# Performance work log

Measured on AMD Instinct MI355X. Metric: run time of the kernel, lower is better.

Reference implementation:

```python
import jax, jax.numpy as jnp
import numpy as np

B, N, D = 16, 2048, 128
NEG = jnp.float32(-2.0**32 + 1)

def setup_inputs() -> dict:
    key = jax.random.key(0)
    ks = jax.random.split(key, 9)
    s = 1.0 / np.sqrt(D)
    return {
        "queries": jax.random.normal(ks[0], (B, N, D), jnp.float32),
        "keys": jax.random.normal(ks[1], (B, N, D), jnp.float32),
        "padding_mask": jax.random.randint(ks[2], (B, N), 0, 2, jnp.int32),
        "Wq": jax.random.uniform(ks[3], (D, D), jnp.float32, -s, s),
        "bq": jax.random.uniform(ks[4], (D,), jnp.float32, -s, s),
        "Wk": jax.random.uniform(ks[5], (D, D), jnp.float32, -s, s),
        "bk": jax.random.uniform(ks[6], (D,), jnp.float32, -s, s),
        "Wv": jax.random.uniform(ks[7], (D, D), jnp.float32, -s, s),
        "bv": jax.random.uniform(ks[8], (D,), jnp.float32, -s, s),
    }

def reference(queries, keys, padding_mask, Wq, bq, Wk, bk, Wv, bv):
    d = queries.shape[-1]
    eq = queries @ Wq.T + bq            # [B,N,D]
    ek = keys @ Wk.T + bk               # [B,N,D]
    ev = keys @ Wv.T + bv               # [B,N,D]
    # scaled scores [B,N,N]
    coefs = jnp.einsum('bnd,bmd->bnm', eq, ek) / jnp.sqrt(jnp.float32(d))
    # key padding: large negative where keys row sums to zero (broadcast over query axis)
    key_pad = (jnp.sum(keys, axis=-1) == 0).astype(jnp.float32) * NEG   # [B,N]
    out = jnp.where(padding_mask[:, None, :] == 0, key_pad[:, None, :], coefs)
    out = jax.nn.softmax(out, axis=2)
    # NOTE: original applies query mask along the KEY axis (unsqueeze(1)) -- kept faithfully
    q_pad = (jnp.sum(queries, axis=-1) != 0).astype(jnp.float32)        # [B,N]
    out = out * q_pad[:, None, :]
    out = jnp.einsum('bnm,bmd->bnd', out, ev)
    return out + queries
```

## Files before the change

kernel.cpp:

```cpp
#include <hip/hip_runtime.h>
#include <hip/hip_bf16.h>


#define SCALE_LOG2E 0.12751875f

typedef __bf16 bf16x8 __attribute__((ext_vector_type(8)));
typedef float  f32x4  __attribute__((ext_vector_type(4)));

static __device__ __forceinline__ float fexp2(float x) {
#if __has_builtin(__builtin_amdgcn_exp2f)
    return __builtin_amdgcn_exp2f(x);
#else
    float r; asm("v_exp_f32 %0, %1" : "=v"(r) : "v"(x)); return r;
#endif
}

__global__ __launch_bounds__(256) void prep_kernel(
    const float* __restrict__ Wq, const float* __restrict__ Wk,
    const float* __restrict__ Wv, __bf16* __restrict__ wb)
{
    int i = blockIdx.x * 256 + threadIdx.x;
    int w = i >> 11, c = i & 2047;
    int col = c & 15, quad = (c >> 4) & 3, f = (c >> 6) & 3, ct = c >> 8;
    const float* src = ((w == 0) ? Wq : (w == 1) ? Wk : Wv)
                       + (size_t)(ct * 16 + col) * 128 + f * 32 + quad * 8;
    float4 a = *(const float4*)src, b = *(const float4*)(src + 4);
    bf16x8 t = {(__bf16)a.x, (__bf16)a.y, (__bf16)a.z, (__bf16)a.w,
                (__bf16)b.x, (__bf16)b.y, (__bf16)b.z, (__bf16)b.w};
    *(bf16x8*)&wb[(size_t)w * 16384 + (size_t)c * 8] = t;
}

__global__ __launch_bounds__(256) void proj_kernel(
    const float* __restrict__ Q, const float* __restrict__ K,
    const int* __restrict__ PM, const __bf16* __restrict__ wb,
    const float* __restrict__ Bq, const float* __restrict__ Bk,
    const float* __restrict__ Bv,
    __bf16* __restrict__ eqb, __bf16* __restrict__ ekf, __bf16* __restrict__ evf,
    float* __restrict__ madd)
{
    __shared__ __bf16 stage[128 * 72];
    const int tid  = threadIdx.x;
    const int wave = tid >> 6, lane = tid & 63;
    const int col  = lane & 15, quad = lane >> 4;
    const int w = blockIdx.x >> 9;
    const int rowbase = (blockIdx.x & 511) * 64;
    const int myrow   = rowbase + wave * 16 + col;
    const int bb   = rowbase >> 11;
    const int m16b = (rowbase & 2047) >> 4;

    const float* asrc = (w == 0) ? Q : K;
    bf16x8 a[4];
    float ss = 0.f;
    #pragma unroll
    for (int f = 0; f < 4; ++f) {
        const float* p = asrc + (size_t)myrow * 128 + f * 32 + quad * 8;
        float4 v0 = *(const float4*)p, v1 = *(const float4*)(p + 4);
        float vv[8] = {v0.x, v0.y, v0.z, v0.w, v1.x, v1.y, v1.z, v1.w};
        #pragma unroll
        for (int j = 0; j < 8; ++j) { ss += vv[j]; a[f][j] = (__bf16)vv[j]; }
    }

    float rm = 1.f;
    if (w == 1) {
        ss += __shfl_xor(ss, 16); ss += __shfl_xor(ss, 32);
        int pmv = PM[myrow];
        rm = (pmv != 0) ? 1.f : 0.f;
        if (quad == 0) madd[myrow] = (pmv == 0 && ss == 0.f) ? -1.0e5f : 0.f;
    } else if (w == 2) {
        float qs = 0.f;
        #pragma unroll
        for (int f = 0; f < 4; ++f) {
            const float* p = Q + (size_t)myrow * 128 + f * 32 + quad * 8;
            float4 v0 = *(const float4*)p, v1 = *(const float4*)(p + 4);
            qs += v0.x + v0.y + v0.z + v0.w + v1.x + v1.y + v1.z + v1.w;
        }
        qs += __shfl_xor(qs, 16); qs += __shfl_xor(qs, 32);
        rm = (qs != 0.f) ? 1.f : 0.f;
    }
    float rmul[4];
    #pragma unroll
    for (int r = 0; r < 4; ++r) rmul[r] = __shfl(rm, quad * 4 + r);

    const float sc = (w == 0) ? SCALE_LOG2E : 1.f;
    const float* bias = (w == 0) ? Bq : (w == 1) ? Bk : Bv;
    const __bf16* wbp = wb + w * 16384;

    f32x4 acc[8];
    #pragma unroll
    for (int ct = 0; ct < 8; ++ct) { f32x4 z = {0.f, 0.f, 0.f, 0.f}; acc[ct] = z; }
    #pragma unroll
    for (int f = 0; f < 4; ++f) {
        #pragma unroll
        for (int ct = 0; ct < 8; ++ct) {
            bf16x8 bfr = *(const bf16x8*)&wbp[(size_t)(ct * 4 + f) * 512 + lane * 8];
            acc[ct] = __builtin_amdgcn_mfma_f32_16x16x32_bf16(a[f], bfr, acc[ct], 0, 0, 0);
        }
    }
    #pragma unroll
    for (int ct = 0; ct < 8; ++ct) {
        float bv = bias[ct * 16 + col];
        #pragma unroll
        for (int r = 0; r < 4; ++r) {
            float v = (acc[ct][r] + bv) * rmul[r] * sc;
            int rr = wave * 16 + quad * 4 + r;
            if (w == 2) stage[(ct * 16 + col) * 72 + rr] = (__bf16)v;
            else        stage[rr * 136 + ct * 16 + col] = (__bf16)v;
        }
    }
    __syncthreads();

    if (w == 0) {
        int r = tid >> 2, seg = (tid & 3) * 32;
        uint4* g4 = (uint4*)(eqb + (size_t)(rowbase + r) * 128 + seg);
        const uint4* s4 = (const uint4*)&stage[r * 136 + seg];
        g4[0] = s4[0]; g4[1] = s4[1]; g4[2] = s4[2]; g4[3] = s4[3];
    } else if (w == 1) {
        __bf16* dst = ekf + (size_t)bb * 2048 * 128 + (size_t)m16b * 2048;
        #pragma unroll
        for (int c = 0; c < 4; ++c) {
            int s = tid + c * 256;
            int l = s & 63, f = (s >> 6) & 3, m = s >> 8;
            *(uint4*)&dst[(size_t)s * 8] =
                *(const uint4*)&stage[(m * 16 + (l & 15)) * 136 + f * 32 + ((l >> 4) & 3) * 8];
        }
    } else {
        __bf16* dst = evf + (size_t)bb * 2048 * 128 + (size_t)(rowbase & 2047) * 128;
        #pragma unroll
        for (int c = 0; c < 4; ++c) {
            int s = tid + c * 256;
            int l = s & 63, dt = (s >> 6) & 7, tl = s >> 9;
            int cl = l & 15, ql = l >> 4;
            uint2 xa = *(const uint2*)&stage[(dt * 16 + cl) * 72 + tl * 32 + ql * 4];
            uint2 xb = *(const uint2*)&stage[(dt * 16 + cl) * 72 + tl * 32 + 16 + ql * 4];
            uint4 v = {xa.x, xa.y, xb.x, xb.y};
            *(uint4*)&dst[(size_t)s * 8] = v;
        }
    }
}

__global__ __launch_bounds__(256, 2) void attn_kernel(
    const __bf16* __restrict__ eqb, const __bf16* __restrict__ ekf,
    const __bf16* __restrict__ evf, const float* __restrict__ madd,
    const float* __restrict__ Q, float* __restrict__ out)
{
    __shared__ struct { float obuf[2][32 * 140]; float lbuf[2][32]; } sm;

    const int tid  = threadIdx.x;
    const int wave = tid >> 6, lane = tid & 63;
    const int col  = lane & 15, quad = lane >> 4;
    const int i  = blockIdx.x;
    const int b  = 2 * (i & 7) + ((i >> 3) & 1);
    const int qt = i >> 4;
    const int rowg0 = b * 2048 + qt * 32;
    const __bf16* ekb_b = ekf + (size_t)b * 2048 * 128;
    const __bf16* evb_b = evf + (size_t)b * 2048 * 128;
    const float*  dmb   = madd + b * 2048;

    bf16x8 aqf[2][4];
    #pragma unroll
    for (int q2 = 0; q2 < 2; ++q2)
        #pragma unroll
        for (int f = 0; f < 4; ++f)
            aqf[q2][f] = *(const bf16x8*)&eqb[(size_t)(rowg0 + q2 * 16 + col) * 128 + f * 32 + quad * 8];

    f32x4 o[2][8];
    float lsum[2] = {0.f, 0.f};
    #pragma unroll
    for (int q2 = 0; q2 < 2; ++q2)
        #pragma unroll
        for (int dt = 0; dt < 8; ++dt) { f32x4 z = {0.f, 0.f, 0.f, 0.f}; o[q2][dt] = z; }

    const int kq0 = wave * 512;

    bf16x8 kc[8], vf[8];
    {
        const int m16 = kq0 >> 4;
        #pragma unroll
        for (int f = 0; f < 4; ++f) {
            kc[f]     = *(const bf16x8*)&ekb_b[(size_t)((m16 + 0) * 4 + f) * 512 + lane * 8];
            kc[4 + f] = *(const bf16x8*)&ekb_b[(size_t)((m16 + 1) * 4 + f) * 512 + lane * 8];
        }
        const int t32 = kq0 >> 5;
        #pragma unroll
        for (int dt = 0; dt < 8; ++dt)
            vf[dt] = *(const bf16x8*)&evb_b[((size_t)t32 * 8 + dt) * 512 + lane * 8];
    }
    float4 dm0 = *(const float4*)&dmb[kq0 + quad * 4];
    float4 dm1 = *(const float4*)&dmb[kq0 + 16 + quad * 4];

    for (int it = 0; it < 16; ++it) {
        const int kb = kq0 + it * 32;

        bf16x8 kn[8], vn[8];
        float4 dn0, dn1;
        if (it < 15) {
            const int m16n = (kb >> 4) + 2;
            #pragma unroll
            for (int f = 0; f < 4; ++f) {
                kn[f]     = *(const bf16x8*)&ekb_b[(size_t)((m16n + 0) * 4 + f) * 512 + lane * 8];
                kn[4 + f] = *(const bf16x8*)&ekb_b[(size_t)((m16n + 1) * 4 + f) * 512 + lane * 8];
            }
            const int t32n = (kb >> 5) + 1;
            #pragma unroll
            for (int dt = 0; dt < 8; ++dt)
                vn[dt] = *(const bf16x8*)&evb_b[((size_t)t32n * 8 + dt) * 512 + lane * 8];
            dn0 = *(const float4*)&dmb[kb + 32 + quad * 4];
            dn1 = *(const float4*)&dmb[kb + 48 + quad * 4];
        }

        f32x4 s[2][2];
        {
            f32x4 i0 = {dm0.x, dm0.y, dm0.z, dm0.w};
            f32x4 i1 = {dm1.x, dm1.y, dm1.z, dm1.w};
            s[0][0] = i0; s[0][1] = i1; s[1][0] = i0; s[1][1] = i1;
        }
        __builtin_amdgcn_s_setprio(1);
        #pragma unroll
        for (int f = 0; f < 4; ++f) {
            #pragma unroll
            for (int q2 = 0; q2 < 2; ++q2) {
                s[q2][0] = __builtin_amdgcn_mfma_f32_16x16x32_bf16(kc[f],     aqf[q2][f], s[q2][0], 0, 0, 0);
                s[q2][1] = __builtin_amdgcn_mfma_f32_16x16x32_bf16(kc[4 + f], aqf[q2][f], s[q2][1], 0, 0, 0);
            }
        }
        __builtin_amdgcn_s_setprio(0);

        bf16x8 pq[2];
        #pragma unroll
        for (int q2 = 0; q2 < 2; ++q2)
            #pragma unroll
            for (int g = 0; g < 2; ++g)
                #pragma unroll
                for (int r = 0; r < 4; ++r) {
                    float e = fexp2(s[q2][g][r]);
                    pq[q2][g * 4 + r] = (__bf16)e;
                    lsum[q2] += e;
                }

        __builtin_amdgcn_s_setprio(1);
        #pragma unroll
        for (int dt = 0; dt < 8; ++dt) {
            #pragma unroll
            for (int q2 = 0; q2 < 2; ++q2)
                o[q2][dt] = __builtin_amdgcn_mfma_f32_16x16x32_bf16(vf[dt], pq[q2], o[q2][dt], 0, 0, 0);
        }
        __builtin_amdgcn_s_setprio(0);

        if (it < 15) {
            #pragma unroll
            for (int f = 0; f < 8; ++f) { kc[f] = kn[f]; vf[f] = vn[f]; }
            dm0 = dn0; dm1 = dn1;
        }
    }

    #pragma unroll
    for (int q2 = 0; q2 < 2; ++q2) {
        lsum[q2] += __shfl_xor(lsum[q2], 16);
        lsum[q2] += __shfl_xor(lsum[q2], 32);
    }

    if (wave & 1) {
        int slot = wave >> 1;
        #pragma unroll
        for (int q2 = 0; q2 < 2; ++q2) {
            #pragma unroll
            for (int dt = 0; dt < 8; ++dt) {
                float4 v = {o[q2][dt][0], o[q2][dt][1], o[q2][dt][2], o[q2][dt][3]};
                *(float4*)&sm.obuf[slot][(q2 * 16 + col) * 140 + dt * 16 + quad * 4] = v;
            }
            if (quad == 0) sm.lbuf[slot][q2 * 16 + col] = lsum[q2];
        }
    }
    __syncthreads();
    if (!(wave & 1)) {
        int slot = wave >> 1;
        #pragma unroll
        for (int q2 = 0; q2 < 2; ++q2) {
            lsum[q2] += sm.lbuf[slot][q2 * 16 + col];
            #pragma unroll
            for (int dt = 0; dt < 8; ++dt) {
                float4 t = *(const float4*)&sm.obuf[slot][(q2 * 16 + col) * 140 + dt * 16 + quad * 4];
                o[q2][dt][0] += t.x; o[q2][dt][1] += t.y;
                o[q2][dt][2] += t.z; o[q2][dt][3] += t.w;
            }
        }
    }
    __syncthreads();
    if (wave == 2) {
        #pragma unroll
        for (int q2 = 0; q2 < 2; ++q2) {
            #pragma unroll
            for (int dt = 0; dt < 8; ++dt) {
                float4 v = {o[q2][dt][0], o[q2][dt][1], o[q2][dt][2], o[q2][dt][3]};
                *(float4*)&sm.obuf[0][(q2 * 16 + col) * 140 + dt * 16 + quad * 4] = v;
            }
            if (quad == 0) sm.lbuf[0][q2 * 16 + col] = lsum[q2];
        }
    }
    __syncthreads();
    if (wave == 0) {
        #pragma unroll
        for (int q2 = 0; q2 < 2; ++q2) {
            float inv = 1.f / (lsum[q2] + sm.lbuf[0][q2 * 16 + col]);
            const size_t rowoff = (size_t)(rowg0 + q2 * 16 + col) * 128;
            #pragma unroll
            for (int dt = 0; dt < 8; ++dt) {
                float4 t = *(const float4*)&sm.obuf[0][(q2 * 16 + col) * 140 + dt * 16 + quad * 4];
                f32x4 qres = __builtin_nontemporal_load((const f32x4*)&Q[rowoff + dt * 16 + quad * 4]);
                f32x4 v;
                v[0] = (o[q2][dt][0] + t.x) * inv + qres[0];
                v[1] = (o[q2][dt][1] + t.y) * inv + qres[1];
                v[2] = (o[q2][dt][2] + t.z) * inv + qres[2];
                v[3] = (o[q2][dt][3] + t.w) * inv + qres[3];
                __builtin_nontemporal_store(v, (f32x4*)&out[rowoff + dt * 16 + quad * 4]);
            }
        }
    }
}

extern "C" void kernel_launch(void* const* d_in, const int* in_sizes, int n_in,
                              void* d_out, int out_size, void* d_ws, size_t ws_size,
                              hipStream_t stream)
{
    const float* Q  = (const float*)d_in[0];
    const float* K  = (const float*)d_in[1];
    const int*   PM = (const int*)d_in[2];
    const float* Wq = (const float*)d_in[3];
    const float* Bq = (const float*)d_in[4];
    const float* Wk = (const float*)d_in[5];
    const float* Bk = (const float*)d_in[6];
    const float* Wv = (const float*)d_in[7];
    const float* Bv = (const float*)d_in[8];
    float* out = (float*)d_out;

    const size_t SZE = (size_t)16 * 2048 * 128;
    __bf16* eqb = (__bf16*)d_ws;
    __bf16* ekf = eqb + SZE;
    __bf16* evf = ekf + SZE;
    float* madd = (float*)(evf + SZE);
    __bf16* wb  = (__bf16*)(madd + 16 * 2048);

    prep_kernel<<<24, 256, 0, stream>>>(Wq, Wk, Wv, wb);
    proj_kernel<<<1536, 256, 0, stream>>>(Q, K, PM, wb, Bq, Bk, Bv,
                                          eqb, ekf, evf, madd);
    attn_kernel<<<1024, 256, 0, stream>>>(eqb, ekf, evf, madd, Q, out);
}
```

Baseline: 160.4 us.

## Fuse Q/K/V projections per block and cut attention register and LDS use

The projection kernel now has each block compute the Q, K and V projections for its 64 rows, rather than launching separate blocks per weight. This reads Q and K once and avoids reloading Q for the query-padding check. The attention kernel drops register double-buffering of V fragments, loading them at the start of each iteration instead, and shrinks the LDS reduction buffer to a single slot with a serialized reduction order. The aim is less global traffic and lower register/LDS pressure for better occupancy, at the cost of exposing V load latency and adding more barriers.

New measurement: 165.8 us. 1.03x slower.

```diff
diff --git a/kernel.cpp b/kernel.cpp
--- a/kernel.cpp
+++ b/kernel.cpp
@@ -42,79 +42,88 @@
     const int tid  = threadIdx.x;
     const int wave = tid >> 6, lane = tid & 63;
     const int col  = lane & 15, quad = lane >> 4;
-    const int w = blockIdx.x >> 9;
-    const int rowbase = (blockIdx.x & 511) * 64;
+    const int rowbase = blockIdx.x * 64;
     const int myrow   = rowbase + wave * 16 + col;
     const int bb   = rowbase >> 11;
     const int m16b = (rowbase & 2047) >> 4;
 
-    const float* asrc = (w == 0) ? Q : K;
-    bf16x8 a[4];
-    float ss = 0.f;
+    bf16x8 aq[4], ak[4];
+    float qs = 0.f, ks = 0.f;
     #pragma unroll
     for (int f = 0; f < 4; ++f) {
-        const float* p = asrc + (size_t)myrow * 128 + f * 32 + quad * 8;
+        const float* p = Q + (size_t)myrow * 128 + f * 32 + quad * 8;
         float4 v0 = *(const float4*)p, v1 = *(const float4*)(p + 4);
         float vv[8] = {v0.x, v0.y, v0.z, v0.w, v1.x, v1.y, v1.z, v1.w};
         #pragma unroll
-        for (int j = 0; j < 8; ++j) { ss += vv[j]; a[f][j] = (__bf16)vv[j]; }
-    }
-
-    float rm = 1.f;
-    if (w == 1) {
-        ss += __shfl_xor(ss, 16); ss += __shfl_xor(ss, 32);
-        int pmv = PM[myrow];
-        rm = (pmv != 0) ? 1.f : 0.f;
-        if (quad == 0) madd[myrow] = (pmv == 0 && ss == 0.f) ? -1.0e5f : 0.f;
-    } else if (w == 2) {
-        float qs = 0.f;
-        #pragma unroll
-        for (int f = 0; f < 4; ++f) {
-            const float* p = Q + (size_t)myrow * 128 + f * 32 + quad * 8;
-            float4 v0 = *(const float4*)p, v1 = *(const float4*)(p + 4);
-            qs += v0.x + v0.y + v0.z + v0.w + v1.x + v1.y + v1.z + v1.w;
-        }
-        qs += __shfl_xor(qs, 16); qs += __shfl_xor(qs, 32);
-        rm = (qs != 0.f) ? 1.f : 0.f;
-    }
-    float rmul[4];
-    #pragma unroll
-    for (int r = 0; r < 4; ++r) rmul[r] = __shfl(rm, quad * 4 + r);
-
-    const float sc = (w == 0) ? SCALE_LOG2E : 1.f;
-    const float* bias = (w == 0) ? Bq : (w == 1) ? Bk : Bv;
-    const __bf16* wbp = wb + w * 16384;
-
-    f32x4 acc[8];
-    #pragma unroll
-    for (int ct = 0; ct < 8; ++ct) { f32x4 z = {0.f, 0.f, 0.f, 0.f}; acc[ct] = z; }
-    #pragma unroll
-    for (int f = 0; f < 4; ++f) {
+        for (int j = 0; j < 8; ++j) { qs += vv[j]; aq[f][j] = (__bf16)vv[j]; }
+        const float* pk = K + (size_t)myrow * 128 + f * 32 + quad * 8;
+        float4 w0 = *(const float4*)pk, w1 = *(const float4*)(pk + 4);
+        float ww[8] = {w0.x, w0.y, w0.z, w0.w, w1.x, w1.y, w1.z, w1.w};
+        #pragma unroll
+        for (int j = 0; j < 8; ++j) { ks += ww[j]; ak[f][j] = (__bf16)ww[j]; }
+    }
+    qs += __shfl_xor(qs, 16); qs += __shfl_xor(qs, 32);
+    ks += __shfl_xor(ks, 16); ks += __shfl_xor(ks, 32);
+    int pmv = PM[myrow];
+    if (quad == 0) madd[myrow] = (pmv == 0 && ks == 0.f) ? -1.0e5f : 0.f;
+    float rmk_s = (pmv != 0) ? 1.f : 0.f;
+    float rmv_s = (qs != 0.f) ? 1.f : 0.f;
+    float rk[4], rv[4];
+    #pragma unroll
+    for (int r = 0; r < 4; ++r) {
+        rk[r] = __shfl(rmk_s, quad * 4 + r);
+        rv[r] = __shfl(rmv_s, quad * 4 + r);
+    }
+
+    {
+        f32x4 acc[8];
+        #pragma unroll
+        for (int ct = 0; ct < 8; ++ct) { f32x4 z = {0.f, 0.f, 0.f, 0.f}; acc[ct] = z; }
+        #pragma unroll
+        for (int f = 0; f < 4; ++f)
+            #pragma unroll
+            for (int ct = 0; ct < 8; ++ct) {
+                bf16x8 bfr = *(const bf16x8*)&wb[(size_t)(ct * 4 + f) * 512 + lane * 8];
+                acc[ct] = __builtin_amdgcn_mfma_f32_16x16x32_bf16(aq[f], bfr, acc[ct], 0, 0, 0);
+            }
         #pragma unroll
         for (int ct = 0; ct < 8; ++ct) {
-            bf16x8 bfr = *(const bf16x8*)&wbp[(size_t)(ct * 4 + f) * 512 + lane * 8];
-            acc[ct] = __builtin_amdgcn_mfma_f32_16x16x32_bf16(a[f], bfr, acc[ct], 0, 0, 0);
-        }
-    }
-    #pragma unroll
-    for (int ct = 0; ct < 8; ++ct) {
-        float bv = bias[ct * 16 + col];
-        #pragma unroll
-        for (int r = 0; r < 4; ++r) {
-            float v = (acc[ct][r] + bv) * rmul[r] * sc;
-            int rr = wave * 16 + quad * 4 + r;
-            if (w == 2) stage[(ct * 16 + col) * 72 + rr] = (__bf16)v;
-            else        stage[rr * 136 + ct * 16 + col] = (__bf16)v;
-        }
-    }
-    __syncthreads();
-
-    if (w == 0) {
+            float bvv = Bq[ct * 16 + col];
+            #pragma unroll
+            for (int r = 0; r < 4; ++r) {
+                int rr = wave * 16 + quad * 4 + r;
+                stage[rr * 136 + ct * 16 + col] = (__bf16)((acc[ct][r] + bvv) * SCALE_LOG2E);
+            }
+        }
+        __syncthreads();
         int r = tid >> 2, seg = (tid & 3) * 32;
         uint4* g4 = (uint4*)(eqb + (size_t)(rowbase + r) * 128 + seg);
         const uint4* s4 = (const uint4*)&stage[r * 136 + seg];
         g4[0] = s4[0]; g4[1] = s4[1]; g4[2] = s4[2]; g4[3] = s4[3];
-    } else if (w == 1) {
+    }
+    __syncthreads();
+
+    {
+        f32x4 acc[8];
+        #pragma unroll
+        for (int ct = 0; ct < 8; ++ct) { f32x4 z = {0.f, 0.f, 0.f, 0.f}; acc[ct] = z; }
+        #pragma unroll
+        for (int f = 0; f < 4; ++f)
+            #pragma unroll
+            for (int ct = 0; ct < 8; ++ct) {
+                bf16x8 bfr = *(const bf16x8*)&wb[(size_t)16384 + (size_t)(ct * 4 + f) * 512 + lane * 8];
+                acc[ct] = __builtin_amdgcn_mfma_f32_16x16x32_bf16(ak[f], bfr, acc[ct], 0, 0, 0);
+            }
+        #pragma unroll
+        for (int ct = 0; ct < 8; ++ct) {
+            float bvv = Bk[ct * 16 + col];
+            #pragma unroll
+            for (int r = 0; r < 4; ++r) {
+                int rr = wave * 16 + quad * 4 + r;
+                stage[rr * 136 + ct * 16 + col] = (__bf16)((acc[ct][r] + bvv) * rk[r]);
+            }
+        }
+        __syncthreads();
         __bf16* dst = ekf + (size_t)bb * 2048 * 128 + (size_t)m16b * 2048;
         #pragma unroll
         for (int c = 0; c < 4; ++c) {
@@ -123,7 +132,30 @@
             *(uint4*)&dst[(size_t)s * 8] =
                 *(const uint4*)&stage[(m * 16 + (l & 15)) * 136 + f * 32 + ((l >> 4) & 3) * 8];
         }
-    } else {
+    }
+    __syncthreads();
+
+    {
+        f32x4 acc[8];
+        #pragma unroll
+        for (int ct = 0; ct < 8; ++ct) { f32x4 z = {0.f, 0.f, 0.f, 0.f}; acc[ct] = z; }
+        #pragma unroll
+        for (int f = 0; f < 4; ++f)
+            #pragma unroll
+            for (int ct = 0; ct < 8; ++ct) {
+                bf16x8 bfr = *(const bf16x8*)&wb[(size_t)32768 + (size_t)(ct * 4 + f) * 512 + lane * 8];
+                acc[ct] = __builtin_amdgcn_mfma_f32_16x16x32_bf16(ak[f], bfr, acc[ct], 0, 0, 0);
+            }
+        #pragma unroll
+        for (int ct = 0; ct < 8; ++ct) {
+            float bvv = Bv[ct * 16 + col];
+            #pragma unroll
+            for (int r = 0; r < 4; ++r) {
+                int rr = wave * 16 + quad * 4 + r;
+                stage[(ct * 16 + col) * 72 + rr] = (__bf16)((acc[ct][r] + bvv) * rv[r]);
+            }
+        }
+        __syncthreads();
         __bf16* dst = evf + (size_t)bb * 2048 * 128 + (size_t)(rowbase & 2047) * 128;
         #pragma unroll
         for (int c = 0; c < 4; ++c) {
@@ -143,7 +175,7 @@
     const __bf16* __restrict__ evf, const float* __restrict__ madd,
     const float* __restrict__ Q, float* __restrict__ out)
 {
-    __shared__ struct { float obuf[2][32 * 140]; float lbuf[2][32]; } sm;
+    __shared__ struct { float obuf[32 * 132]; float lbuf[2][32]; } sm;
 
     const int tid  = threadIdx.x;
     const int wave = tid >> 6, lane = tid & 63;
@@ -172,7 +204,7 @@
 
     const int kq0 = wave * 512;
 
-    bf16x8 kc[8], vf[8];
+    bf16x8 kc[8];
     {
         const int m16 = kq0 >> 4;
         #pragma unroll
@@ -180,18 +212,20 @@
             kc[f]     = *(const bf16x8*)&ekb_b[(size_t)((m16 + 0) * 4 + f) * 512 + lane * 8];
             kc[4 + f] = *(const bf16x8*)&ekb_b[(size_t)((m16 + 1) * 4 + f) * 512 + lane * 8];
         }
-        const int t32 = kq0 >> 5;
+    }
+    float4 dm0 = *(const float4*)&dmb[kq0 + quad * 4];
+    float4 dm1 = *(const float4*)&dmb[kq0 + 16 + quad * 4];
+
+    for (int it = 0; it < 16; ++it) {
+        const int kb = kq0 + it * 32;
+        const int t32 = kb >> 5;
+
+        bf16x8 vf[8];
         #pragma unroll
         for (int dt = 0; dt < 8; ++dt)
             vf[dt] = *(const bf16x8*)&evb_b[((size_t)t32 * 8 + dt) * 512 + lane * 8];
-    }
-    float4 dm0 = *(const float4*)&dmb[kq0 + quad * 4];
-    float4 dm1 = *(const float4*)&dmb[kq0 + 16 + quad * 4];
-
-    for (int it = 0; it < 16; ++it) {
-        const int kb = kq0 + it * 32;
-
-        bf16x8 kn[8], vn[8];
+
+        bf16x8 kn[8];
         float4 dn0, dn1;
         if (it < 15) {
             const int m16n = (kb >> 4) + 2;
@@ -200,10 +234,6 @@
                 kn[f]     = *(const bf16x8*)&ekb_b[(size_t)((m16n + 0) * 4 + f) * 512 + lane * 8];
                 kn[4 + f] = *(const bf16x8*)&ekb_b[(size_t)((m16n + 1) * 4 + f) * 512 + lane * 8];
             }
-            const int t32n = (kb >> 5) + 1;
-            #pragma unroll
-            for (int dt = 0; dt < 8; ++dt)
-                vn[dt] = *(const bf16x8*)&evb_b[((size_t)t32n * 8 + dt) * 512 + lane * 8];
             dn0 = *(const float4*)&dmb[kb + 32 + quad * 4];
             dn1 = *(const float4*)&dmb[kb + 48 + quad * 4];
         }
@@ -248,7 +278,7 @@
 
         if (it < 15) {
             #pragma unroll
-            for (int f = 0; f < 8; ++f) { kc[f] = kn[f]; vf[f] = vn[f]; }
+            for (int f = 0; f < 8; ++f) kc[f] = kn[f];
             dm0 = dn0; dm1 = dn1;
         }
     }
@@ -259,40 +289,53 @@
         lsum[q2] += __shfl_xor(lsum[q2], 32);
     }
 
-    if (wave & 1) {
-        int slot = wave >> 1;
+    if (wave == 1) {
         #pragma unroll
         for (int q2 = 0; q2 < 2; ++q2) {
             #pragma unroll
             for (int dt = 0; dt < 8; ++dt) {
                 float4 v = {o[q2][dt][0], o[q2][dt][1], o[q2][dt][2], o[q2][dt][3]};
-                *(float4*)&sm.obuf[slot][(q2 * 16 + col) * 140 + dt * 16 + quad * 4] = v;
-            }
-            if (quad == 0) sm.lbuf[slot][q2 * 16 + col] = lsum[q2];
-        }
-    }
-    __syncthreads();
-    if (!(wave & 1)) {
-        int slot = wave >> 1;
-        #pragma unroll
-        for (int q2 = 0; q2 < 2; ++q2) {
-            lsum[q2] += sm.lbuf[slot][q2 * 16 + col];
-            #pragma unroll
-            for (int dt = 0; dt < 8; ++dt) {
-                float4 t = *(const float4*)&sm.obuf[slot][(q2 * 16 + col) * 140 + dt * 16 + quad * 4];
+                *(float4*)&sm.obuf[(q2 * 16 + col) * 132 + dt * 16 + quad * 4] = v;
+            }
+            if (quad == 0) sm.lbuf[0][q2 * 16 + col] = lsum[q2];
+        }
+    }
+    __syncthreads();
+    if (wave == 0) {
+        #pragma unroll
+        for (int q2 = 0; q2 < 2; ++q2) {
+            lsum[q2] += sm.lbuf[0][q2 * 16 + col];
+            #pragma unroll
+            for (int dt = 0; dt < 8; ++dt) {
+                float4 t = *(const float4*)&sm.obuf[(q2 * 16 + col) * 132 + dt * 16 + quad * 4];
                 o[q2][dt][0] += t.x; o[q2][dt][1] += t.y;
                 o[q2][dt][2] += t.z; o[q2][dt][3] += t.w;
             }
         }
     }
     __syncthreads();
+    if (wave == 3) {
+        #pragma unroll
+        for (int q2 = 0; q2 < 2; ++q2) {
+            #pragma unroll
+            for (int dt = 0; dt < 8; ++dt) {
+                float4 v = {o[q2][dt][0], o[q2][dt][1], o[q2][dt][2], o[q2][dt][3]};
+                *(float4*)&sm.obuf[(q2 * 16 + col) * 132 + dt * 16 + quad * 4] = v;
+            }
+            if (quad == 0) sm.lbuf[1][q2 * 16 + col] = lsum[q2];
+        }
+    }
+    __syncthreads();
     if (wave == 2) {
         #pragma unroll
         for (int q2 = 0; q2 < 2; ++q2) {
-            #pragma unroll
-            for (int dt = 0; dt < 8; ++dt) {
-                float4 v = {o[q2][dt][0], o[q2][dt][1], o[q2][dt][2], o[q2][dt][3]};
-                *(float4*)&sm.obuf[0][(q2 * 16 + col) * 140 + dt * 16 + quad * 4] = v;
+            lsum[q2] += sm.lbuf[1][q2 * 16 + col];
+            #pragma unroll
+            for (int dt = 0; dt < 8; ++dt) {
+                float4 t = *(const float4*)&sm.obuf[(q2 * 16 + col) * 132 + dt * 16 + quad * 4];
+                float4 v = {o[q2][dt][0] + t.x, o[q2][dt][1] + t.y,
+                            o[q2][dt][2] + t.z, o[q2][dt][3] + t.w};
+                *(float4*)&sm.obuf[(q2 * 16 + col) * 132 + dt * 16 + quad * 4] = v;
             }
             if (quad == 0) sm.lbuf[0][q2 * 16 + col] = lsum[q2];
         }
@@ -305,7 +348,7 @@
             const size_t rowoff = (size_t)(rowg0 + q2 * 16 + col) * 128;
             #pragma unroll
             for (int dt = 0; dt < 8; ++dt) {
-                float4 t = *(const float4*)&sm.obuf[0][(q2 * 16 + col) * 140 + dt * 16 + quad * 4];
+                float4 t = *(const float4*)&sm.obuf[(q2 * 16 + col) * 132 + dt * 16 + quad * 4];
                 f32x4 qres = __builtin_nontemporal_load((const f32x4*)&Q[rowoff + dt * 16 + quad * 4]);
                 f32x4 v;
                 v[0] = (o[q2][dt][0] + t.x) * inv + qres[0];
@@ -341,7 +384,7 @@
     __bf16* wb  = (__bf16*)(madd + 16 * 2048);
 
     prep_kernel<<<24, 256, 0, stream>>>(Wq, Wk, Wv, wb);
-    proj_kernel<<<1536, 256, 0, stream>>>(Q, K, PM, wb, Bq, Bk, Bv,
-                                          eqb, ekf, evf, madd);
+    proj_kernel<<<512, 256, 0, stream>>>(Q, K, PM, wb, Bq, Bk, Bv,
+                                         eqb, ekf, evf, madd);
     attn_kernel<<<1024, 256, 0, stream>>>(eqb, ekf, evf, madd, Q, out);
 }
```

## Give each wave its own query rows and drop the cross-wave LDS reduction

Applied to the files above, without the earlier changes.

Previously each block handled 32 query rows and split the key axis across its 4 waves, then merged partial outputs and row sums through shared memory with three barriers. Now each wave owns 16 distinct query rows and walks all 2048 keys, so no LDS reduction or syncs are needed, and the grid halves to 512 blocks. K fragments are double-buffered by ping-ponging two register sets across unrolled steps, while V is loaded just before use. The trade-off is that each wave reads four times more K/V per query row with fewer concurrent waves, and V loads are no longer prefetched ahead of the MFMAs.

New measurement: 178.8 us. +11.5%, slower.

```diff
diff --git a/kernel.cpp b/kernel.cpp
--- a/kernel.cpp
+++ b/kernel.cpp
@@ -138,183 +138,116 @@
     }
 }
 
+static __device__ __forceinline__ void attn_step(
+    int it, const __bf16* __restrict__ ekb_b, const __bf16* __restrict__ evb_b,
+    const float* __restrict__ dmb, int lane, int quad,
+    const bf16x8 aqf[4], bf16x8 kcur[8], float4 dmc0, float4 dmc1,
+    bf16x8 knext[8], float4& dmn0, float4& dmn1,
+    f32x4 o[8], float& lsum)
+{
+    bf16x8 vf[8];
+    #pragma unroll
+    for (int dt = 0; dt < 8; ++dt)
+        vf[dt] = *(const bf16x8*)&evb_b[((size_t)it * 8 + dt) * 512 + lane * 8];
+
+    if (it < 63) {
+        const int m16n = (it + 1) * 2;
+        #pragma unroll
+        for (int f = 0; f < 4; ++f) {
+            knext[f]     = *(const bf16x8*)&ekb_b[(size_t)((m16n + 0) * 4 + f) * 512 + lane * 8];
+            knext[4 + f] = *(const bf16x8*)&ekb_b[(size_t)((m16n + 1) * 4 + f) * 512 + lane * 8];
+        }
+        dmn0 = *(const float4*)&dmb[(it + 1) * 32 + quad * 4];
+        dmn1 = *(const float4*)&dmb[(it + 1) * 32 + 16 + quad * 4];
+    }
+
+    f32x4 s0 = {dmc0.x, dmc0.y, dmc0.z, dmc0.w};
+    f32x4 s1 = {dmc1.x, dmc1.y, dmc1.z, dmc1.w};
+    __builtin_amdgcn_s_setprio(1);
+    #pragma unroll
+    for (int f = 0; f < 4; ++f) {
+        s0 = __builtin_amdgcn_mfma_f32_16x16x32_bf16(kcur[f],     aqf[f], s0, 0, 0, 0);
+        s1 = __builtin_amdgcn_mfma_f32_16x16x32_bf16(kcur[4 + f], aqf[f], s1, 0, 0, 0);
+    }
+    __builtin_amdgcn_s_setprio(0);
+
+    bf16x8 pq;
+    #pragma unroll
+    for (int r = 0; r < 4; ++r) {
+        float e = fexp2(s0[r]);
+        pq[r] = (__bf16)e;
+        lsum += e;
+    }
+    #pragma unroll
+    for (int r = 0; r < 4; ++r) {
+        float e = fexp2(s1[r]);
+        pq[4 + r] = (__bf16)e;
+        lsum += e;
+    }
+
+    __builtin_amdgcn_s_setprio(1);
+    #pragma unroll
+    for (int dt = 0; dt < 8; ++dt)
+        o[dt] = __builtin_amdgcn_mfma_f32_16x16x32_bf16(vf[dt], pq, o[dt], 0, 0, 0);
+    __builtin_amdgcn_s_setprio(0);
+}
+
 __global__ __launch_bounds__(256, 2) void attn_kernel(
     const __bf16* __restrict__ eqb, const __bf16* __restrict__ ekf,
     const __bf16* __restrict__ evf, const float* __restrict__ madd,
     const float* __restrict__ Q, float* __restrict__ out)
 {
-    __shared__ struct { float obuf[2][32 * 140]; float lbuf[2][32]; } sm;
-
     const int tid  = threadIdx.x;
     const int wave = tid >> 6, lane = tid & 63;
     const int col  = lane & 15, quad = lane >> 4;
     const int i  = blockIdx.x;
     const int b  = 2 * (i & 7) + ((i >> 3) & 1);
     const int qt = i >> 4;
-    const int rowg0 = b * 2048 + qt * 32;
+    const int rowg0 = b * 2048 + qt * 64 + wave * 16;
     const __bf16* ekb_b = ekf + (size_t)b * 2048 * 128;
     const __bf16* evb_b = evf + (size_t)b * 2048 * 128;
     const float*  dmb   = madd + b * 2048;
 
-    bf16x8 aqf[2][4];
-    #pragma unroll
-    for (int q2 = 0; q2 < 2; ++q2)
-        #pragma unroll
-        for (int f = 0; f < 4; ++f)
-            aqf[q2][f] = *(const bf16x8*)&eqb[(size_t)(rowg0 + q2 * 16 + col) * 128 + f * 32 + quad * 8];
-
-    f32x4 o[2][8];
-    float lsum[2] = {0.f, 0.f};
-    #pragma unroll
-    for (int q2 = 0; q2 < 2; ++q2)
-        #pragma unroll
-        for (int dt = 0; dt < 8; ++dt) { f32x4 z = {0.f, 0.f, 0.f, 0.f}; o[q2][dt] = z; }
-
-    const int kq0 = wave * 512;
-
-    bf16x8 kc[8], vf[8];
-    {
-        const int m16 = kq0 >> 4;
-        #pragma unroll
-        for (int f = 0; f < 4; ++f) {
-            kc[f]     = *(const bf16x8*)&ekb_b[(size_t)((m16 + 0) * 4 + f) * 512 + lane * 8];
-            kc[4 + f] = *(const bf16x8*)&ekb_b[(size_t)((m16 + 1) * 4 + f) * 512 + lane * 8];
-        }
-        const int t32 = kq0 >> 5;
-        #pragma unroll
-        for (int dt = 0; dt < 8; ++dt)
-            vf[dt] = *(const bf16x8*)&evb_b[((size_t)t32 * 8 + dt) * 512 + lane * 8];
-    }
-    float4 dm0 = *(const float4*)&dmb[kq0 + quad * 4];
-    float4 dm1 = *(const float4*)&dmb[kq0 + 16 + quad * 4];
-
-    for (int it = 0; it < 16; ++it) {
-        const int kb = kq0 + it * 32;
-
-        bf16x8 kn[8], vn[8];
-        float4 dn0, dn1;
-        if (it < 15) {
-            const int m16n = (kb >> 4) + 2;
-            #pragma unroll
-            for (int f = 0; f < 4; ++f) {
-                kn[f]     = *(const bf16x8*)&ekb_b[(size_t)((m16n + 0) * 4 + f) * 512 + lane * 8];
-                kn[4 + f] = *(const bf16x8*)&ekb_b[(size_t)((m16n + 1) * 4 + f) * 512 + lane * 8];
-            }
-            const int t32n = (kb >> 5) + 1;
-            #pragma unroll
-            for (int dt = 0; dt < 8; ++dt)
-                vn[dt] = *(const bf16x8*)&evb_b[((size_t)t32n * 8 + dt) * 512 + lane * 8];
-            dn0 = *(const float4*)&dmb[kb + 32 + quad * 4];
-            dn1 = *(const float4*)&dmb[kb + 48 + quad * 4];
-        }
-
-        f32x4 s[2][2];
-        {
-            f32x4 i0 = {dm0.x, dm0.y, dm0.z, dm0.w};
-            f32x4 i1 = {dm1.x, dm1.y, dm1.z, dm1.w};
-            s[0][0] = i0; s[0][1] = i1; s[1][0] = i0; s[1][1] = i1;
-        }
-        __builtin_amdgcn_s_setprio(1);
-        #pragma unroll
-        for (int f = 0; f < 4; ++f) {
-            #pragma unroll
-            for (int q2 = 0; q2 < 2; ++q2) {
-                s[q2][0] = __builtin_amdgcn_mfma_f32_16x16x32_bf16(kc[f],     aqf[q2][f], s[q2][0], 0, 0, 0);
-                s[q2][1] = __builtin_amdgcn_mfma_f32_16x16x32_bf16(kc[4 + f], aqf[q2][f], s[q2][1], 0, 0, 0);
-            }
-        }
-        __builtin_amdgcn_s_setprio(0);
-
-        bf16x8 pq[2];
-        #pragma unroll
-        for (int q2 = 0; q2 < 2; ++q2)
-            #pragma unroll
-            for (int g = 0; g < 2; ++g)
-                #pragma unroll
-                for (int r = 0; r < 4; ++r) {
-                    float e = fexp2(s[q2][g][r]);
-                    pq[q2][g * 4 + r] = (__bf16)e;
-                    lsum[q2] += e;
-                }
-
-        __builtin_amdgcn_s_setprio(1);
-        #pragma unroll
-        for (int dt = 0; dt < 8; ++dt) {
-            #pragma unroll
-            for (int q2 = 0; q2 < 2; ++q2)
-                o[q2][dt] = __builtin_amdgcn_mfma_f32_16x16x32_bf16(vf[dt], pq[q2], o[q2][dt], 0, 0, 0);
-        }
-        __builtin_amdgcn_s_setprio(0);
-
-        if (it < 15) {
-            #pragma unroll
-            for (int f = 0; f < 8; ++f) { kc[f] = kn[f]; vf[f] = vn[f]; }
-            dm0 = dn0; dm1 = dn1;
-        }
-    }
-
-    #pragma unroll
-    for (int q2 = 0; q2 < 2; ++q2) {
-        lsum[q2] += __shfl_xor(lsum[q2], 16);
-        lsum[q2] += __shfl_xor(lsum[q2], 32);
-    }
-
-    if (wave & 1) {
-        int slot = wave >> 1;
-        #pragma unroll
-        for (int q2 = 0; q2 < 2; ++q2) {
-            #pragma unroll
-            for (int dt = 0; dt < 8; ++dt) {
-                float4 v = {o[q2][dt][0], o[q2][dt][1], o[q2][dt][2], o[q2][dt][3]};
-                *(float4*)&sm.obuf[slot][(q2 * 16 + col) * 140 + dt * 16 + quad * 4] = v;
-            }
-            if (quad == 0) sm.lbuf[slot][q2 * 16 + col] = lsum[q2];
-        }
-    }
-    __syncthreads();
-    if (!(wave & 1)) {
-        int slot = wave >> 1;
-        #pragma unroll
-        for (int q2 = 0; q2 < 2; ++q2) {
-            lsum[q2] += sm.lbuf[slot][q2 * 16 + col];
-            #pragma unroll
-            for (int dt = 0; dt < 8; ++dt) {
-                float4 t = *(const float4*)&sm.obuf[slot][(q2 * 16 + col) * 140 + dt * 16 + quad * 4];
-                o[q2][dt][0] += t.x; o[q2][dt][1] += t.y;
-                o[q2][dt][2] += t.z; o[q2][dt][3] += t.w;
-            }
-        }
-    }
-    __syncthreads();
-    if (wave == 2) {
-        #pragma unroll
-        for (int q2 = 0; q2 < 2; ++q2) {
-            #pragma unroll
-            for (int dt = 0; dt < 8; ++dt) {
-                float4 v = {o[q2][dt][0], o[q2][dt][1], o[q2][dt][2], o[q2][dt][3]};
-                *(float4*)&sm.obuf[0][(q2 * 16 + col) * 140 + dt * 16 + quad * 4] = v;
-            }
-            if (quad == 0) sm.lbuf[0][q2 * 16 + col] = lsum[q2];
-        }
-    }
-    __syncthreads();
-    if (wave == 0) {
-        #pragma unroll
-        for (int q2 = 0; q2 < 2; ++q2) {
-            float inv = 1.f / (lsum[q2] + sm.lbuf[0][q2 * 16 + col]);
-            const size_t rowoff = (size_t)(rowg0 + q2 * 16 + col) * 128;
-            #pragma unroll
-            for (int dt = 0; dt < 8; ++dt) {
-                float4 t = *(const float4*)&sm.obuf[0][(q2 * 16 + col) * 140 + dt * 16 + quad * 4];
-                f32x4 qres = __builtin_nontemporal_load((const f32x4*)&Q[rowoff + dt * 16 + quad * 4]);
-                f32x4 v;
-                v[0] = (o[q2][dt][0] + t.x) * inv + qres[0];
-                v[1] = (o[q2][dt][1] + t.y) * inv + qres[1];
-                v[2] = (o[q2][dt][2] + t.z) * inv + qres[2];
-                v[3] = (o[q2][dt][3] + t.w) * inv + qres[3];
-                __builtin_nontemporal_store(v, (f32x4*)&out[rowoff + dt * 16 + quad * 4]);
-            }
-        }
+    bf16x8 aqf[4];
+    #pragma unroll
+    for (int f = 0; f < 4; ++f)
+        aqf[f] = *(const bf16x8*)&eqb[(size_t)(rowg0 + col) * 128 + f * 32 + quad * 8];
+
+    f32x4 o[8];
+    float lsum = 0.f;
+    #pragma unroll
+    for (int dt = 0; dt < 8; ++dt) { f32x4 z = {0.f, 0.f, 0.f, 0.f}; o[dt] = z; }
+
+    bf16x8 kA[8], kB[8];
+    float4 dA0, dA1, dB0 = {0, 0, 0, 0}, dB1 = {0, 0, 0, 0};
+    #pragma unroll
+    for (int f = 0; f < 4; ++f) {
+        kA[f]     = *(const bf16x8*)&ekb_b[(size_t)(0 * 4 + f) * 512 + lane * 8];
+        kA[4 + f] = *(const bf16x8*)&ekb_b[(size_t)(1 * 4 + f) * 512 + lane * 8];
+    }
+    dA0 = *(const float4*)&dmb[quad * 4];
+    dA1 = *(const float4*)&dmb[16 + quad * 4];
+
+    for (int it2 = 0; it2 < 32; ++it2) {
+        attn_step(2 * it2,     ekb_b, evb_b, dmb, lane, quad, aqf,
+                  kA, dA0, dA1, kB, dB0, dB1, o, lsum);
+        attn_step(2 * it2 + 1, ekb_b, evb_b, dmb, lane, quad, aqf,
+                  kB, dB0, dB1, kA, dA0, dA1, o, lsum);
+    }
+
+    lsum += __shfl_xor(lsum, 16);
+    lsum += __shfl_xor(lsum, 32);
+    float inv = 1.f / lsum;
+    const size_t rowoff = (size_t)(rowg0 + col) * 128;
+    #pragma unroll
+    for (int dt = 0; dt < 8; ++dt) {
+        f32x4 qres = __builtin_nontemporal_load((const f32x4*)&Q[rowoff + dt * 16 + quad * 4]);
+        f32x4 v;
+        v[0] = o[dt][0] * inv + qres[0];
+        v[1] = o[dt][1] * inv + qres[1];
+        v[2] = o[dt][2] * inv + qres[2];
+        v[3] = o[dt][3] * inv + qres[3];
+        __builtin_nontemporal_store(v, (f32x4*)&out[rowoff + dt * 16 + quad * 4]);
     }
 }
 
@@ -343,5 +276,5 @@
     prep_kernel<<<24, 256, 0, stream>>>(Wq, Wk, Wv, wb);
     proj_kernel<<<1536, 256, 0, stream>>>(Q, K, PM, wb, Bq, Bk, Bv,
                                           eqb, ekf, evf, madd);
-    attn_kernel<<<1024, 256, 0, stream>>>(eqb, ekf, evf, madd, Q, out);
-}
+    attn_kernel<<<512, 256, 0, stream>>>(eqb, ekf, evf, madd, Q, out);
+}
```

## Use 512-thread attention blocks covering 64 query rows and load V without prefetch

Applied to the files above, without the earlier changes.

The attention kernel now runs 512 threads per block: two groups of four waves, each group handling 32 query rows over split key ranges. The grid is halved to 512 blocks. V fragments are no longer double-buffered across iterations and are loaded at the start of each iteration instead, which lowers register pressure enough for the 512-thread, 2-blocks-per-CU launch bound. The cross-wave reduction is reworked into a two-level pairwise tree with a smaller LDS row pitch. The risk is exposed V load latency now that the prefetch is gone, plus extra barrier cost across the larger block.

After: 166.3 us. 1.04x slower.

```diff
diff --git a/kernel.cpp b/kernel.cpp
--- a/kernel.cpp
+++ b/kernel.cpp
@@ -138,20 +138,21 @@
     }
 }
 
-__global__ __launch_bounds__(256, 2) void attn_kernel(
+__global__ __launch_bounds__(512, 2) void attn_kernel(
     const __bf16* __restrict__ eqb, const __bf16* __restrict__ ekf,
     const __bf16* __restrict__ evf, const float* __restrict__ madd,
     const float* __restrict__ Q, float* __restrict__ out)
 {
-    __shared__ struct { float obuf[2][32 * 140]; float lbuf[2][32]; } sm;
+    __shared__ struct { float obuf[2][32 * 132]; float lbuf[2][2][32]; } sm;
 
     const int tid  = threadIdx.x;
     const int wave = tid >> 6, lane = tid & 63;
+    const int lw   = wave & 3, qh = wave >> 2;
     const int col  = lane & 15, quad = lane >> 4;
     const int i  = blockIdx.x;
     const int b  = 2 * (i & 7) + ((i >> 3) & 1);
     const int qt = i >> 4;
-    const int rowg0 = b * 2048 + qt * 32;
+    const int rowg0 = b * 2048 + qt * 64 + qh * 32;
     const __bf16* ekb_b = ekf + (size_t)b * 2048 * 128;
     const __bf16* evb_b = evf + (size_t)b * 2048 * 128;
     const float*  dmb   = madd + b * 2048;
@@ -170,9 +171,9 @@
         #pragma unroll
         for (int dt = 0; dt < 8; ++dt) { f32x4 z = {0.f, 0.f, 0.f, 0.f}; o[q2][dt] = z; }
 
-    const int kq0 = wave * 512;
-
-    bf16x8 kc[8], vf[8];
+    const int kq0 = lw * 512;
+
+    bf16x8 kc[8];
     {
         const int m16 = kq0 >> 4;
         #pragma unroll
@@ -180,18 +181,20 @@
             kc[f]     = *(const bf16x8*)&ekb_b[(size_t)((m16 + 0) * 4 + f) * 512 + lane * 8];
             kc[4 + f] = *(const bf16x8*)&ekb_b[(size_t)((m16 + 1) * 4 + f) * 512 + lane * 8];
         }
-        const int t32 = kq0 >> 5;
+    }
+    float4 dm0 = *(const float4*)&dmb[kq0 + quad * 4];
+    float4 dm1 = *(const float4*)&dmb[kq0 + 16 + quad * 4];
+
+    for (int it = 0; it < 16; ++it) {
+        const int kb = kq0 + it * 32;
+        const int t32 = kb >> 5;
+
+        bf16x8 vf[8];
         #pragma unroll
         for (int dt = 0; dt < 8; ++dt)
             vf[dt] = *(const bf16x8*)&evb_b[((size_t)t32 * 8 + dt) * 512 + lane * 8];
-    }
-    float4 dm0 = *(const float4*)&dmb[kq0 + quad * 4];
-    float4 dm1 = *(const float4*)&dmb[kq0 + 16 + quad * 4];
-
-    for (int it = 0; it < 16; ++it) {
-        const int kb = kq0 + it * 32;
-
-        bf16x8 kn[8], vn[8];
+
+        bf16x8 kn[8];
         float4 dn0, dn1;
         if (it < 15) {
             const int m16n = (kb >> 4) + 2;
@@ -200,10 +203,6 @@
                 kn[f]     = *(const bf16x8*)&ekb_b[(size_t)((m16n + 0) * 4 + f) * 512 + lane * 8];
                 kn[4 + f] = *(const bf16x8*)&ekb_b[(size_t)((m16n + 1) * 4 + f) * 512 + lane * 8];
             }
-            const int t32n = (kb >> 5) + 1;
-            #pragma unroll
-            for (int dt = 0; dt < 8; ++dt)
-                vn[dt] = *(const bf16x8*)&evb_b[((size_t)t32n * 8 + dt) * 512 + lane * 8];
             dn0 = *(const float4*)&dmb[kb + 32 + quad * 4];
             dn1 = *(const float4*)&dmb[kb + 48 + quad * 4];
         }
@@ -248,7 +247,7 @@
 
         if (it < 15) {
             #pragma unroll
-            for (int f = 0; f < 8; ++f) { kc[f] = kn[f]; vf[f] = vn[f]; }
+            for (int f = 0; f < 8; ++f) kc[f] = kn[f];
             dm0 = dn0; dm1 = dn1;
         }
     }
@@ -259,53 +258,66 @@
         lsum[q2] += __shfl_xor(lsum[q2], 32);
     }
 
-    if (wave & 1) {
-        int slot = wave >> 1;
+    if (lw == 1) {
         #pragma unroll
         for (int q2 = 0; q2 < 2; ++q2) {
             #pragma unroll
             for (int dt = 0; dt < 8; ++dt) {
                 float4 v = {o[q2][dt][0], o[q2][dt][1], o[q2][dt][2], o[q2][dt][3]};
-                *(float4*)&sm.obuf[slot][(q2 * 16 + col) * 140 + dt * 16 + quad * 4] = v;
-            }
-            if (quad == 0) sm.lbuf[slot][q2 * 16 + col] = lsum[q2];
-        }
-    }
-    __syncthreads();
-    if (!(wave & 1)) {
-        int slot = wave >> 1;
-        #pragma unroll
-        for (int q2 = 0; q2 < 2; ++q2) {
-            lsum[q2] += sm.lbuf[slot][q2 * 16 + col];
-            #pragma unroll
-            for (int dt = 0; dt < 8; ++dt) {
-                float4 t = *(const float4*)&sm.obuf[slot][(q2 * 16 + col) * 140 + dt * 16 + quad * 4];
+                *(float4*)&sm.obuf[qh][(q2 * 16 + col) * 132 + dt * 16 + quad * 4] = v;
+            }
+            if (quad == 0) sm.lbuf[qh][0][q2 * 16 + col] = lsum[q2];
+        }
+    }
+    __syncthreads();
+    if (lw == 0) {
+        #pragma unroll
+        for (int q2 = 0; q2 < 2; ++q2) {
+            lsum[q2] += sm.lbuf[qh][0][q2 * 16 + col];
+            #pragma unroll
+            for (int dt = 0; dt < 8; ++dt) {
+                float4 t = *(const float4*)&sm.obuf[qh][(q2 * 16 + col) * 132 + dt * 16 + quad * 4];
                 o[q2][dt][0] += t.x; o[q2][dt][1] += t.y;
                 o[q2][dt][2] += t.z; o[q2][dt][3] += t.w;
             }
         }
     }
     __syncthreads();
-    if (wave == 2) {
+    if (lw == 3) {
         #pragma unroll
         for (int q2 = 0; q2 < 2; ++q2) {
             #pragma unroll
             for (int dt = 0; dt < 8; ++dt) {
                 float4 v = {o[q2][dt][0], o[q2][dt][1], o[q2][dt][2], o[q2][dt][3]};
-                *(float4*)&sm.obuf[0][(q2 * 16 + col) * 140 + dt * 16 + quad * 4] = v;
-            }
-            if (quad == 0) sm.lbuf[0][q2 * 16 + col] = lsum[q2];
-        }
-    }
-    __syncthreads();
-    if (wave == 0) {
-        #pragma unroll
-        for (int q2 = 0; q2 < 2; ++q2) {
-            float inv = 1.f / (lsum[q2] + sm.lbuf[0][q2 * 16 + col]);
+                *(float4*)&sm.obuf[qh][(q2 * 16 + col) * 132 + dt * 16 + quad * 4] = v;
+            }
+            if (quad == 0) sm.lbuf[qh][1][q2 * 16 + col] = lsum[q2];
+        }
+    }
+    __syncthreads();
+    if (lw == 2) {
+        #pragma unroll
+        for (int q2 = 0; q2 < 2; ++q2) {
+            lsum[q2] += sm.lbuf[qh][1][q2 * 16 + col];
+            #pragma unroll
+            for (int dt = 0; dt < 8; ++dt) {
+                float4 t = *(const float4*)&sm.obuf[qh][(q2 * 16 + col) * 132 + dt * 16 + quad * 4];
+                float4 v = {o[q2][dt][0] + t.x, o[q2][dt][1] + t.y,
+                            o[q2][dt][2] + t.z, o[q2][dt][3] + t.w};
+                *(float4*)&sm.obuf[qh][(q2 * 16 + col) * 132 + dt * 16 + quad * 4] = v;
+            }
+            if (quad == 0) sm.lbuf[qh][0][q2 * 16 + col] = lsum[q2];
+        }
+    }
+    __syncthreads();
+    if (lw == 0) {
+        #pragma unroll
+        for (int q2 = 0; q2 < 2; ++q2) {
+            float inv = 1.f / (lsum[q2] + sm.lbuf[qh][0][q2 * 16 + col]);
             const size_t rowoff = (size_t)(rowg0 + q2 * 16 + col) * 128;
             #pragma unroll
             for (int dt = 0; dt < 8; ++dt) {
-                float4 t = *(const float4*)&sm.obuf[0][(q2 * 16 + col) * 140 + dt * 16 + quad * 4];
+                float4 t = *(const float4*)&sm.obuf[qh][(q2 * 16 + col) * 132 + dt * 16 + quad * 4];
                 f32x4 qres = __builtin_nontemporal_load((const f32x4*)&Q[rowoff + dt * 16 + quad * 4]);
                 f32x4 v;
                 v[0] = (o[q2][dt][0] + t.x) * inv + qres[0];
@@ -343,5 +355,5 @@
     prep_kernel<<<24, 256, 0, stream>>>(Wq, Wk, Wv, wb);
     proj_kernel<<<1536, 256, 0, stream>>>(Q, K, PM, wb, Bq, Bk, Bv,
                                           eqb, ekf, evf, madd);
-    attn_kernel<<<1024, 256, 0, stream>>>(eqb, ekf, evf, madd, Q, out);
-}
+    attn_kernel<<<512, 512, 0, stream>>>(eqb, ekf, evf, madd, Q, out);
+}
```
